# Kernel tuning notes

Measured on AMD Instinct MI355X. Metric: run time of the kernel, lower is better.

Reference implementation:

```python
import jax, jax.numpy as jnp
import numpy as np

N_NODES = 100000
N_EDGES = 1600000
F_IN = 256
F_OUT = 128


def setup_inputs() -> dict:
    key = jax.random.key(0)
    k_x, k_row, k_col, k_v, k_w = jax.random.split(key, 5)
    x = jax.random.normal(k_x, (N_NODES, F_IN), dtype=jnp.float32)
    row = jax.random.randint(k_row, (N_EDGES,), 0, N_NODES, dtype=jnp.int32)
    col = jax.random.randint(k_col, (N_EDGES,), 0, N_NODES, dtype=jnp.int32)
    vals = jax.random.uniform(k_v, (N_EDGES,), dtype=jnp.float32)
    # glorot init for weights_0 [F_IN, F_OUT]
    limit = np.sqrt(6.0 / (F_IN + F_OUT)).astype(np.float32)
    W = jax.random.uniform(k_w, (F_IN, F_OUT), minval=-limit, maxval=limit, dtype=jnp.float32)
    b = jnp.zeros((F_OUT,), dtype=jnp.float32)
    return {"x": x, "W": W, "b": b, "vals": vals, "row": row, "col": col}


def reference(x, W, b, vals, row, col):
    # dropout rate is 0.0 -> identity (tf.nn.dropout(x, keep_prob=1.0))
    pre_sup = x @ W  # [N, F_OUT] dense feature projection
    # SpMM: output[i] = sum_e (vals[e] * pre_sup[col[e]]) for edges with row[e] == i
    msgs = vals[:, None] * pre_sup[col]  # [E, F_OUT] gather + scale
    out = jax.ops.segment_sum(msgs, row, num_segments=N_NODES)  # scatter-add
    return jax.nn.relu(out + b)
```

## Files before the change

kernel.cpp:

```cpp
#include <hip/hip_runtime.h>
#include <hip/hip_bf16.h>

#define N_NODES 100000
#define N_EDGES 1600000
#define F_IN 256
#define F_OUT 128
#define SCAN_BLOCKS ((N_NODES + 255) / 256)

#define N_BINS 128
#define RPB 782
#define L1_BLOCKS 256
#define L1_THREADS 512
#define L1_EDGES (N_EDGES / L1_BLOCKS)
#define CNT_SIZE (N_BINS * L1_BLOCKS)

typedef __attribute__((ext_vector_type(8))) short short8;
typedef __attribute__((ext_vector_type(4))) float f32x4;
typedef __attribute__((ext_vector_type(2))) float f32x2;
typedef __attribute__((ext_vector_type(2))) unsigned int uint2v;

static __device__ __forceinline__ unsigned short bf16b(float f) {
    __hip_bfloat16 h = __float2bfloat16(f);
    return *reinterpret_cast<unsigned short*>(&h);
}

__global__ void wprep_kernel(const float* __restrict__ W, unsigned short* __restrict__ Wsw) {
    int idx = blockIdx.x * 256 + threadIdx.x;
    int e  = idx & 7;
    int col = (idx >> 3) & 127;
    int kk = (idx >> 10) & 3;
    int ks = idx >> 12;
    int k = ks * 32 + kk * 8 + e;
    Wsw[idx] = bf16b(W[k * 128 + col]);
}

__global__ __launch_bounds__(64) void gemm_kernel(const float* __restrict__ x,
                                                  const unsigned short* __restrict__ Wsw,
                                                  unsigned short* __restrict__ preb) {
    __shared__ char sx[16384];
    const int lane = threadIdx.x;
    const int m0 = blockIdx.x * 16;
    const int l15 = lane & 15;
    const int kk = lane >> 4;

#pragma unroll
    for (int j = 0; j < 16; ++j) {
        const char* gsrc = reinterpret_cast<const char*>(x + (size_t)(m0 + j) * F_IN)
                         + ((lane ^ j) << 4);
        __builtin_amdgcn_global_load_lds(
            (const __attribute__((address_space(1))) void*)gsrc,
            (__attribute__((address_space(3))) void*)(sx + j * 1024),
            16, 0, 0);
    }
    __syncthreads();

    f32x4 acc[8];
#pragma unroll
    for (int i = 0; i < 8; ++i) acc[i] = (f32x4){0.f, 0.f, 0.f, 0.f};

    const char* swb = sx + l15 * 1024;
    const int sw = l15 << 4;
#pragma unroll
    for (int ks = 0; ks < 8; ++ks) {
        const int cb = ks * 128 + kk * 32;
        float4 fa = *reinterpret_cast<const float4*>(swb + ((cb) ^ sw));
        float4 fb = *reinterpret_cast<const float4*>(swb + ((cb + 16) ^ sw));
        short8 a;
        a[0] = (short)bf16b(fa.x); a[1] = (short)bf16b(fa.y);
        a[2] = (short)bf16b(fa.z); a[3] = (short)bf16b(fa.w);
        a[4] = (short)bf16b(fb.x); a[5] = (short)bf16b(fb.y);
        a[6] = (short)bf16b(fb.z); a[7] = (short)bf16b(fb.w);
        const short8* wv = reinterpret_cast<const short8*>(Wsw) + ((ks * 4 + kk) * 128 + l15);
#pragma unroll
        for (int nf = 0; nf < 8; ++nf) {
            short8 b = wv[nf * 16];
            acc[nf] = __builtin_amdgcn_mfma_f32_16x16x32_bf16(a, b, acc[nf], 0, 0, 0);
        }
    }

    const int rbase = m0 + (lane >> 4) * 4;
#pragma unroll
    for (int nf = 0; nf < 8; ++nf) {
        int cc = nf * 16 + l15;
#pragma unroll
        for (int reg = 0; reg < 4; ++reg) {
            preb[(long)(rbase + reg) * F_OUT + cc] = bf16b(acc[nf][reg]);
        }
    }
}

__global__ __launch_bounds__(L1_THREADS) void passA_kernel(const int* __restrict__ row,
                                                           int* __restrict__ cnt) {
    __shared__ int h[N_BINS];
    if (threadIdx.x < N_BINS) h[threadIdx.x] = 0;
    __syncthreads();
    const int g = blockIdx.x;
    const int base = g * L1_EDGES;
    for (int i = threadIdx.x; i < L1_EDGES; i += L1_THREADS) {
        int r = __builtin_nontemporal_load(row + base + i);
        atomicAdd(&h[r / RPB], 1);
    }
    __syncthreads();
    if (threadIdx.x < N_BINS)
        cnt[threadIdx.x * L1_BLOCKS + g] = h[threadIdx.x];
}

__global__ void scan32768_kernel(const int* __restrict__ cnt, int* __restrict__ off) {
    __shared__ int tmp[1024];
    int t = threadIdx.x;
    const int4* c4 = reinterpret_cast<const int4*>(cnt);
    int sum = 0;
#pragma unroll
    for (int j = 0; j < 8; ++j) {
        int4 v = c4[t * 8 + j];
        sum += v.x + v.y + v.z + v.w;
    }
    tmp[t] = sum;
    __syncthreads();
#pragma unroll
    for (int o = 1; o < 1024; o <<= 1) {
        int u = (t >= o) ? tmp[t - o] : 0;
        __syncthreads();
        tmp[t] += u;
        __syncthreads();
    }
    int base = tmp[t] - sum;
#pragma unroll
    for (int j = 0; j < 8; ++j) {
        int4 v = c4[t * 8 + j];
        off[t * 32 + j * 4 + 0] = base; base += v.x;
        off[t * 32 + j * 4 + 1] = base; base += v.y;
        off[t * 32 + j * 4 + 2] = base; base += v.z;
        off[t * 32 + j * 4 + 3] = base; base += v.w;
    }
    if (t == 1023) off[CNT_SIZE] = base;
}

__global__ __launch_bounds__(L1_THREADS) void passB_kernel(const int* __restrict__ row,
                                                           const int* __restrict__ col,
                                                           const float* __restrict__ vals,
                                                           const int* __restrict__ off,
                                                           unsigned* __restrict__ packed,
                                                           unsigned short* __restrict__ valh) {
    __shared__ int cur[N_BINS];
    const int g = blockIdx.x;
    if (threadIdx.x < N_BINS) cur[threadIdx.x] = off[threadIdx.x * L1_BLOCKS + g];
    __syncthreads();
    const int base = g * L1_EDGES;
    for (int i = threadIdx.x; i < L1_EDGES; i += L1_THREADS) {
        int e = base + i;
        int r = __builtin_nontemporal_load(row + e);
        int c = __builtin_nontemporal_load(col + e);
        float v = __builtin_nontemporal_load(vals + e);
        int bin = r / RPB;
        int lr = r - bin * RPB;
        int pos = atomicAdd(&cur[bin], 1);
        packed[pos] = (unsigned)c | ((unsigned)lr << 17);
        valh[pos] = bf16b(v);
    }
}

__global__ __launch_bounds__(1024) void bin_deg_kernel(const unsigned* __restrict__ packed,
                                                       const int* __restrict__ off,
                                                       int* __restrict__ deg) {
    __shared__ int h[RPB];
    const int b = blockIdx.x;
    const int rbase = b * RPB;
    const int nrows = min(RPB, N_NODES - rbase);
    for (int i = threadIdx.x; i < nrows; i += 1024) h[i] = 0;
    __syncthreads();
    const int lo = off[b * L1_BLOCKS];
    const int hi = off[(b + 1) * L1_BLOCKS];
    for (int i = lo + (int)threadIdx.x; i < hi; i += 1024) {
        unsigned p = __builtin_nontemporal_load(packed + i);
        atomicAdd(&h[p >> 17], 1);
    }
    __syncthreads();
    for (int i = threadIdx.x; i < nrows; i += 1024) deg[rbase + i] = h[i];
}

__global__ void scan_block_kernel(const int* __restrict__ deg, int* __restrict__ row_start,
                                  int* __restrict__ bsums) {
    __shared__ int tmp[256];
    int t = threadIdx.x;
    int i = blockIdx.x * 256 + t;
    int d = (i < N_NODES) ? deg[i] : 0;
    tmp[t] = d;
    __syncthreads();
#pragma unroll
    for (int o = 1; o < 256; o <<= 1) {
        int v = (t >= o) ? tmp[t - o] : 0;
        __syncthreads();
        tmp[t] += v;
        __syncthreads();
    }
    if (i < N_NODES) row_start[i] = tmp[t] - d;
    if (t == 255) bsums[blockIdx.x] = tmp[255];
}

__global__ void scan_bsums_kernel(int* __restrict__ bsums) {
    __shared__ int tmp[512];
    int t = threadIdx.x;
    int v = (t < SCAN_BLOCKS) ? bsums[t] : 0;
    tmp[t] = v;
    __syncthreads();
#pragma unroll
    for (int o = 1; o < 512; o <<= 1) {
        int u = (t >= o) ? tmp[t - o] : 0;
        __syncthreads();
        tmp[t] += u;
        __syncthreads();
    }
    bsums[t] = tmp[t] - v;
}

__global__ void scan_add_kernel(int* __restrict__ row_start, const int* __restrict__ bsums) {
    int i = blockIdx.x * 256 + threadIdx.x;
    if (i < N_NODES) {
        row_start[i] = row_start[i] + bsums[blockIdx.x];
        if (i == N_NODES - 1) row_start[N_NODES] = N_EDGES;
    }
}

__global__ __launch_bounds__(1024) void csr_place_kernel(const unsigned* __restrict__ packed,
                                                         const unsigned short* __restrict__ valh,
                                                         const int* __restrict__ off,
                                                         const int* __restrict__ row_start,
                                                         uint2v* __restrict__ edges) {
    __shared__ int cur[RPB];
    const int b = blockIdx.x;
    const int rbase = b * RPB;
    const int nrows = min(RPB, N_NODES - rbase);
    for (int i = threadIdx.x; i < nrows; i += 1024) cur[i] = row_start[rbase + i];
    __syncthreads();
    const int lo = off[b * L1_BLOCKS];
    const int hi = off[(b + 1) * L1_BLOCKS];
    for (int i = lo + (int)threadIdx.x; i < hi; i += 1024) {
        unsigned p = __builtin_nontemporal_load(packed + i);
        unsigned short vh = __builtin_nontemporal_load(valh + i);
        int lr = (int)(p >> 17);
        int c = (int)(p & 0x1FFFFu);
        int pos = atomicAdd(&cur[lr], 1);
        edges[pos] = (uint2v){(unsigned)c, ((unsigned)vh) << 16};
    }
}

__global__ __launch_bounds__(256) void spmm_csr_kernel(
    const unsigned short* __restrict__ preb, const int* __restrict__ row_start,
    const uint2v* __restrict__ edges, const float* __restrict__ bias,
    float* __restrict__ out) {
    const int lane = threadIdx.x & 63;
    const int r = blockIdx.x * 4 + (threadIdx.x >> 6);
    const int s = row_start[r];
    const int t = row_start[r + 1];
    const int n = t - s;
    float a0 = 0.f, a1 = 0.f;

    const char* pb = reinterpret_cast<const char*>(preb);
    const unsigned laneoff = (unsigned)(lane << 2);

    uint2v ev = (uint2v){0u, 0u};
    if (lane < n) ev = edges[s + lane];
    const int nn = n < 64 ? n : 64;
    for (int j0 = 0; j0 < nn; j0 += 8) {
#pragma unroll
        for (int jj = 0; jj < 8; ++jj) {
            int j = j0 + jj;
            unsigned c = (unsigned)__builtin_amdgcn_readlane((int)ev.x, j);
            float v = __uint_as_float((unsigned)__builtin_amdgcn_readlane((int)ev.y, j));
            const char* pbase = pb + ((size_t)c << 8);
            unsigned g = *reinterpret_cast<const unsigned*>(pbase + laneoff);
            a0 += v * __uint_as_float(g << 16);
            a1 += v * __uint_as_float(g & 0xFFFF0000u);
        }
    }
    for (int e = s + 64; e < t; ++e) {
        uint2v cv = edges[e];
        float v = __uint_as_float(cv.y);
        const char* pbase = pb + ((size_t)cv.x << 8);
        unsigned g = *reinterpret_cast<const unsigned*>(pbase + laneoff);
        a0 += v * __uint_as_float(g << 16);
        a1 += v * __uint_as_float(g & 0xFFFF0000u);
    }

    float2 bb = *reinterpret_cast<const float2*>(bias + lane * 2);
    f32x2 o;
    o.x = fmaxf(a0 + bb.x, 0.f);
    o.y = fmaxf(a1 + bb.y, 0.f);
    __builtin_nontemporal_store(o, reinterpret_cast<f32x2*>(out + (size_t)r * F_OUT + lane * 2));
}

extern "C" void kernel_launch(void* const* d_in, const int* in_sizes, int n_in,
                              void* d_out, int out_size, void* d_ws, size_t ws_size,
                              hipStream_t stream) {
    const float* x    = (const float*)d_in[0];
    const float* W    = (const float*)d_in[1];
    const float* b    = (const float*)d_in[2];
    const float* vals = (const float*)d_in[3];
    const int*   row  = (const int*)d_in[4];
    const int*   col  = (const int*)d_in[5];
    float* out = (float*)d_out;

    char* ws = (char*)d_ws;
    unsigned short* preb      = (unsigned short*)(ws);
    unsigned short* Wsw       = (unsigned short*)(ws + 25600000);
    int*            row_start = (int*)(ws + 25665536);
    int*            deg       = (int*)(ws + 26065568);
    int*            bsums     = (int*)(ws + 26465568);
    int*            cnt       = (int*)(ws + 26469664);
    int*            off       = (int*)(ws + 26600736);
    unsigned*       packed    = (unsigned*)(ws + 26731904);
    unsigned short* valh      = (unsigned short*)(ws + 33131904);
    uint2v*         edges     = (uint2v*)(ws + 36331904);

    wprep_kernel<<<128, 256, 0, stream>>>(W, Wsw);
    gemm_kernel<<<N_NODES / 16, 64, 0, stream>>>(x, Wsw, preb);

    passA_kernel<<<L1_BLOCKS, L1_THREADS, 0, stream>>>(row, cnt);
    scan32768_kernel<<<1, 1024, 0, stream>>>(cnt, off);
    passB_kernel<<<L1_BLOCKS, L1_THREADS, 0, stream>>>(row, col, vals, off, packed, valh);

    bin_deg_kernel<<<N_BINS, 1024, 0, stream>>>(packed, off, deg);
    scan_block_kernel<<<SCAN_BLOCKS, 256, 0, stream>>>(deg, row_start, bsums);
    scan_bsums_kernel<<<1, 512, 0, stream>>>(bsums);
    scan_add_kernel<<<SCAN_BLOCKS, 256, 0, stream>>>(row_start, bsums);

    csr_place_kernel<<<N_BINS, 1024, 0, stream>>>(packed, valh, off, row_start, edges);

    spmm_csr_kernel<<<N_NODES / 4, 256, 0, stream>>>(preb, row_start, edges, b, out);
}
```

Baseline: 169.2 us.

## Fuse per-bin degree count, row scan and CSR placement into one kernel

Replaces the bin degree histogram, the three-kernel global prefix scan and the CSR placement kernel with a single per-bin kernel. It counts degrees in shared memory, scans them locally and offsets by the bin start from the existing bin offsets, then places edges. This removes four kernel launches and the global deg/bsums round trips, and the packed array is now read twice inside one block (likely hitting cache). The cost is a 1024-wide block scan with 20 barriers and only 128 blocks doing the placement work.

Result: faster. 160.6 us (-5.1%).

```diff
diff --git a/kernel.cpp b/kernel.cpp
--- a/kernel.cpp
+++ b/kernel.cpp
@@ -5,7 +5,6 @@
 #define N_EDGES 1600000
 #define F_IN 256
 #define F_OUT 128
-#define SCAN_BLOCKS ((N_NODES + 255) / 256)
 
 #define N_BINS 128
 #define RPB 782
@@ -160,88 +159,44 @@
     }
 }
 
-__global__ __launch_bounds__(1024) void bin_deg_kernel(const unsigned* __restrict__ packed,
-                                                       const int* __restrict__ off,
-                                                       int* __restrict__ deg) {
-    __shared__ int h[RPB];
+__global__ __launch_bounds__(1024) void csr_fused_kernel(const unsigned* __restrict__ packed,
+                                                         const unsigned short* __restrict__ valh,
+                                                         const int* __restrict__ off,
+                                                         int* __restrict__ row_start,
+                                                         uint2v* __restrict__ edges) {
+    __shared__ int tmp[1024];
     const int b = blockIdx.x;
+    const int t = threadIdx.x;
     const int rbase = b * RPB;
     const int nrows = min(RPB, N_NODES - rbase);
-    for (int i = threadIdx.x; i < nrows; i += 1024) h[i] = 0;
-    __syncthreads();
     const int lo = off[b * L1_BLOCKS];
     const int hi = off[(b + 1) * L1_BLOCKS];
-    for (int i = lo + (int)threadIdx.x; i < hi; i += 1024) {
-        unsigned p = __builtin_nontemporal_load(packed + i);
-        atomicAdd(&h[p >> 17], 1);
-    }
-    __syncthreads();
-    for (int i = threadIdx.x; i < nrows; i += 1024) deg[rbase + i] = h[i];
-}
-
-__global__ void scan_block_kernel(const int* __restrict__ deg, int* __restrict__ row_start,
-                                  int* __restrict__ bsums) {
-    __shared__ int tmp[256];
-    int t = threadIdx.x;
-    int i = blockIdx.x * 256 + t;
-    int d = (i < N_NODES) ? deg[i] : 0;
-    tmp[t] = d;
-    __syncthreads();
-#pragma unroll
-    for (int o = 1; o < 256; o <<= 1) {
-        int v = (t >= o) ? tmp[t - o] : 0;
-        __syncthreads();
-        tmp[t] += v;
-        __syncthreads();
-    }
-    if (i < N_NODES) row_start[i] = tmp[t] - d;
-    if (t == 255) bsums[blockIdx.x] = tmp[255];
-}
-
-__global__ void scan_bsums_kernel(int* __restrict__ bsums) {
-    __shared__ int tmp[512];
-    int t = threadIdx.x;
-    int v = (t < SCAN_BLOCKS) ? bsums[t] : 0;
-    tmp[t] = v;
-    __syncthreads();
-#pragma unroll
-    for (int o = 1; o < 512; o <<= 1) {
+
+    tmp[t] = 0;
+    __syncthreads();
+    for (int i = lo + t; i < hi; i += 1024)
+        atomicAdd(&tmp[packed[i] >> 17], 1);
+    __syncthreads();
+
+    int d = tmp[t];
+#pragma unroll
+    for (int o = 1; o < 1024; o <<= 1) {
         int u = (t >= o) ? tmp[t - o] : 0;
         __syncthreads();
         tmp[t] += u;
         __syncthreads();
     }
-    bsums[t] = tmp[t] - v;
-}
-
-__global__ void scan_add_kernel(int* __restrict__ row_start, const int* __restrict__ bsums) {
-    int i = blockIdx.x * 256 + threadIdx.x;
-    if (i < N_NODES) {
-        row_start[i] = row_start[i] + bsums[blockIdx.x];
-        if (i == N_NODES - 1) row_start[N_NODES] = N_EDGES;
-    }
-}
-
-__global__ __launch_bounds__(1024) void csr_place_kernel(const unsigned* __restrict__ packed,
-                                                         const unsigned short* __restrict__ valh,
-                                                         const int* __restrict__ off,
-                                                         const int* __restrict__ row_start,
-                                                         uint2v* __restrict__ edges) {
-    __shared__ int cur[RPB];
-    const int b = blockIdx.x;
-    const int rbase = b * RPB;
-    const int nrows = min(RPB, N_NODES - rbase);
-    for (int i = threadIdx.x; i < nrows; i += 1024) cur[i] = row_start[rbase + i];
-    __syncthreads();
-    const int lo = off[b * L1_BLOCKS];
-    const int hi = off[(b + 1) * L1_BLOCKS];
-    for (int i = lo + (int)threadIdx.x; i < hi; i += 1024) {
-        unsigned p = __builtin_nontemporal_load(packed + i);
-        unsigned short vh = __builtin_nontemporal_load(valh + i);
-        int lr = (int)(p >> 17);
-        int c = (int)(p & 0x1FFFFu);
-        int pos = atomicAdd(&cur[lr], 1);
-        edges[pos] = (uint2v){(unsigned)c, ((unsigned)vh) << 16};
+    int excl = lo + tmp[t] - d;
+    if (t < nrows) row_start[rbase + t] = excl;
+    if (b == N_BINS - 1 && t == 0) row_start[N_NODES] = N_EDGES;
+    tmp[t] = excl;
+    __syncthreads();
+
+    for (int i = lo + t; i < hi; i += 1024) {
+        unsigned p = packed[i];
+        unsigned short vh = valh[i];
+        int pos = atomicAdd(&tmp[p >> 17], 1);
+        edges[pos] = (uint2v){p & 0x1FFFFu, ((unsigned)vh) << 16};
     }
 }
 
@@ -305,8 +260,6 @@
     unsigned short* preb      = (unsigned short*)(ws);
     unsigned short* Wsw       = (unsigned short*)(ws + 25600000);
     int*            row_start = (int*)(ws + 25665536);
-    int*            deg       = (int*)(ws + 26065568);
-    int*            bsums     = (int*)(ws + 26465568);
     int*            cnt       = (int*)(ws + 26469664);
     int*            off       = (int*)(ws + 26600736);
     unsigned*       packed    = (unsigned*)(ws + 26731904);
@@ -320,12 +273,7 @@
     scan32768_kernel<<<1, 1024, 0, stream>>>(cnt, off);
     passB_kernel<<<L1_BLOCKS, L1_THREADS, 0, stream>>>(row, col, vals, off, packed, valh);
 
-    bin_deg_kernel<<<N_BINS, 1024, 0, stream>>>(packed, off, deg);
-    scan_block_kernel<<<SCAN_BLOCKS, 256, 0, stream>>>(deg, row_start, bsums);
-    scan_bsums_kernel<<<1, 512, 0, stream>>>(bsums);
-    scan_add_kernel<<<SCAN_BLOCKS, 256, 0, stream>>>(row_start, bsums);
-
-    csr_place_kernel<<<N_BINS, 1024, 0, stream>>>(packed, valh, off, row_start, edges);
+    csr_fused_kernel<<<N_BINS, 1024, 0, stream>>>(packed, valh, off, row_start, edges);
 
     spmm_csr_kernel<<<N_NODES / 4, 256, 0, stream>>>(preb, row_start, edges, b, out);
 }
```
